# Kernel optimization log

Hardware: AMD Instinct MI355X
Metric: run time of the kernel (lower is better)

Reference implementation:

```python
import jax, jax.numpy as jnp
import numpy as np

B, T, D, O = 4, 1024, 256, 256


def setup_inputs() -> dict:
    key = jax.random.key(0)
    kx, kw = jax.random.split(key)
    x = jax.random.normal(kx, (B, T, D), dtype=jnp.float32)
    # he_normal init: stddev = sqrt(2 / fan_in), stacked per-position kernels [T, D, O]
    W = jax.random.normal(kw, (T, D, O), dtype=jnp.float32) * np.sqrt(2.0 / D).astype(np.float32)
    return {"x": x, "W": W}


def reference(x, W):
    # Original loop: out[:, i, :] = mean_{t<=i} (x[:, t, :] @ W[i])
    # = (cumulative mean of x along T) @ per-position kernel W[i].
    t = x.shape[1]
    counts = jnp.arange(1, t + 1, dtype=x.dtype)[:, None]  # (T,1)
    cm = jnp.cumsum(x, axis=1) / counts                    # (B,T,D) cumulative mean
    return jnp.einsum('btd,tdo->bto', cm, W)               # (B,T,O)
```

## Files before the change

kernel.cpp:

```cpp
#include <hip/hip_runtime.h>

#define B_ 4
#define T_ 1024
#define D_ 256
#define O_ 256
#define NC 32
#define CL 32

__global__ __launch_bounds__(256) void chunk_sums(const float* __restrict__ x,
                                                  float* __restrict__ S) {
    const int d  = threadIdx.x;
    const int bc = blockIdx.x;
    const int b  = bc / NC;
    const int c  = bc % NC;
    const float* xp = x + ((size_t)b * T_ + (size_t)c * CL) * D_ + d;
    float s = 0.f;
#pragma unroll
    for (int i = 0; i < CL; ++i) s += xp[(size_t)i * D_];
    S[((size_t)b * NC + c) * D_ + d] = s;
}

__global__ __launch_bounds__(256) void cumsum_mean(const float* __restrict__ x,
                                                   const float* __restrict__ S,
                                                   float* __restrict__ cm) {
    const int d  = threadIdx.x;
    const int bc = blockIdx.x;
    const int b  = bc / NC;
    const int c  = bc % NC;
    float off = 0.f;
    for (int cc = 0; cc < c; ++cc) off += S[((size_t)b * NC + cc) * D_ + d];
    const float* xp = x  + ((size_t)b * T_ + (size_t)c * CL) * D_ + d;
    float*       cp = cm + ((size_t)b * T_ + (size_t)c * CL) * D_ + d;
    float run = off;
#pragma unroll 4
    for (int i = 0; i < CL; ++i) {
        run += xp[(size_t)i * D_];
        const int t = c * CL + i;
        cp[(size_t)i * D_] = run / (float)(t + 1);
    }
}

__global__ __launch_bounds__(256) void gemm_t(const float* __restrict__ cm,
                                              const float* __restrict__ W,
                                              float* __restrict__ out) {
    const int t   = blockIdx.x;
    const int tid = threadIdx.x;
    const int oq  = tid & 63;
    const int dc  = tid >> 6;

    __shared__ float cml[D_][4];
    __shared__ float red[4][64][17];

#pragma unroll
    for (int b = 0; b < 4; ++b)
        cml[tid][b] = cm[((size_t)b * T_ + t) * D_ + tid];
    __syncthreads();

    const float* Wp = W + ((size_t)t * D_ + (size_t)dc * 64) * O_ + (size_t)oq * 4;

    float4 a0 = make_float4(0.f, 0.f, 0.f, 0.f);
    float4 a1 = a0, a2 = a0, a3 = a0;

#pragma unroll 8
    for (int i = 0; i < 64; ++i) {
        const float4 w  = *(const float4*)(Wp + (size_t)i * O_);
        const float4 c4 = *(const float4*)cml[dc * 64 + i];
        a0.x += c4.x * w.x; a0.y += c4.x * w.y; a0.z += c4.x * w.z; a0.w += c4.x * w.w;
        a1.x += c4.y * w.x; a1.y += c4.y * w.y; a1.z += c4.y * w.z; a1.w += c4.y * w.w;
        a2.x += c4.z * w.x; a2.y += c4.z * w.y; a2.z += c4.z * w.z; a2.w += c4.z * w.w;
        a3.x += c4.w * w.x; a3.y += c4.w * w.y; a3.z += c4.w * w.z; a3.w += c4.w * w.w;
    }

    float* r = red[dc][oq];
    r[ 0] = a0.x; r[ 1] = a0.y; r[ 2] = a0.z; r[ 3] = a0.w;
    r[ 4] = a1.x; r[ 5] = a1.y; r[ 6] = a1.z; r[ 7] = a1.w;
    r[ 8] = a2.x; r[ 9] = a2.y; r[10] = a2.z; r[11] = a2.w;
    r[12] = a3.x; r[13] = a3.y; r[14] = a3.z; r[15] = a3.w;
    __syncthreads();

    if (tid < 64) {
        float v[16];
#pragma unroll
        for (int k = 0; k < 16; ++k)
            v[k] = red[0][tid][k] + red[1][tid][k] + red[2][tid][k] + red[3][tid][k];
#pragma unroll
        for (int b = 0; b < 4; ++b) {
            float4 o4 = make_float4(v[b * 4 + 0], v[b * 4 + 1], v[b * 4 + 2], v[b * 4 + 3]);
            *(float4*)&out[((size_t)b * T_ + t) * O_ + (size_t)tid * 4] = o4;
        }
    }
}

extern "C" void kernel_launch(void* const* d_in, const int* in_sizes, int n_in,
                              void* d_out, int out_size, void* d_ws, size_t ws_size,
                              hipStream_t stream) {
    const float* x = (const float*)d_in[0];
    const float* W = (const float*)d_in[1];
    float* out = (float*)d_out;

    float* cm = (float*)d_ws;
    float* S  = (float*)d_ws + (size_t)B_ * T_ * D_;

    chunk_sums <<<B_ * NC, 256, 0, stream>>>(x, S);
    cumsum_mean<<<B_ * NC, 256, 0, stream>>>(x, S, cm);
    gemm_t     <<<T_,      256, 0, stream>>>(cm, W, out);
}
```

Before: 374.3 us.

## Restructure per-position GEMM: one wavefront per timestep, double-buffered nontemporal W loads

The GEMM kernel now gives each 64-thread wavefront a whole timestep over the full D reduction, with four timesteps per block. This removes the shared-memory cross-wave reduction and its second barrier. Weight rows are software-pipelined through a 16-register double buffer using nontemporal loads, and outputs are written with nontemporal stores. The cumsum offset loop is fully unrolled with predication. The cost is more register pressure and a grid of only 256 blocks, which may limit latency hiding on a bandwidth-bound 256 MB weight stream.

```diff
diff --git a/kernel.cpp b/kernel.cpp
--- a/kernel.cpp
+++ b/kernel.cpp
@@ -6,6 +6,8 @@
 #define O_ 256
 #define NC 32
 #define CL 32
+
+typedef float v4f __attribute__((ext_vector_type(4)));
 
 __global__ __launch_bounds__(256) void chunk_sums(const float* __restrict__ x,
                                                   float* __restrict__ S) {
@@ -28,7 +30,11 @@
     const int b  = bc / NC;
     const int c  = bc % NC;
     float off = 0.f;
-    for (int cc = 0; cc < c; ++cc) off += S[((size_t)b * NC + cc) * D_ + d];
+#pragma unroll
+    for (int cc = 0; cc < NC; ++cc) {
+        const float v = S[((size_t)b * NC + cc) * D_ + d];
+        off += (cc < c) ? v : 0.f;
+    }
     const float* xp = x  + ((size_t)b * T_ + (size_t)c * CL) * D_ + d;
     float*       cp = cm + ((size_t)b * T_ + (size_t)c * CL) * D_ + d;
     float run = off;
@@ -43,52 +49,57 @@
 __global__ __launch_bounds__(256) void gemm_t(const float* __restrict__ cm,
                                               const float* __restrict__ W,
                                               float* __restrict__ out) {
-    const int t   = blockIdx.x;
+    const int t0  = blockIdx.x * 4;
     const int tid = threadIdx.x;
+    const int tq  = tid >> 6;
     const int oq  = tid & 63;
-    const int dc  = tid >> 6;
 
-    __shared__ float cml[D_][4];
-    __shared__ float red[4][64][17];
+    __shared__ float cml[4][D_][4];
 
 #pragma unroll
-    for (int b = 0; b < 4; ++b)
-        cml[tid][b] = cm[((size_t)b * T_ + t) * D_ + tid];
+    for (int q = 0; q < 4; ++q)
+#pragma unroll
+        for (int b = 0; b < 4; ++b)
+            cml[q][tid][b] = cm[((size_t)b * T_ + t0 + q) * D_ + tid];
     __syncthreads();
 
-    const float* Wp = W + ((size_t)t * D_ + (size_t)dc * 64) * O_ + (size_t)oq * 4;
+    const v4f* Wp = (const v4f*)(W + (size_t)(t0 + tq) * D_ * O_) + oq;
 
-    float4 a0 = make_float4(0.f, 0.f, 0.f, 0.f);
-    float4 a1 = a0, a2 = a0, a3 = a0;
+    v4f a0 = (v4f)(0.f), a1 = (v4f)(0.f), a2 = (v4f)(0.f), a3 = (v4f)(0.f);
 
-#pragma unroll 8
-    for (int i = 0; i < 64; ++i) {
-        const float4 w  = *(const float4*)(Wp + (size_t)i * O_);
-        const float4 c4 = *(const float4*)cml[dc * 64 + i];
-        a0.x += c4.x * w.x; a0.y += c4.x * w.y; a0.z += c4.x * w.z; a0.w += c4.x * w.w;
-        a1.x += c4.y * w.x; a1.y += c4.y * w.y; a1.z += c4.y * w.z; a1.w += c4.y * w.w;
-        a2.x += c4.z * w.x; a2.y += c4.z * w.y; a2.z += c4.z * w.z; a2.w += c4.z * w.w;
-        a3.x += c4.w * w.x; a3.y += c4.w * w.y; a3.z += c4.w * w.z; a3.w += c4.w * w.w;
+    v4f w[16];
+#pragma unroll
+    for (int j = 0; j < 8; ++j)
+        w[j] = __builtin_nontemporal_load(Wp + (size_t)j * (O_ / 4));
+
+#pragma unroll 1
+    for (int dd = 0; dd < D_; dd += 16) {
+#pragma unroll
+        for (int j = 0; j < 8; ++j)
+            w[8 + j] = __builtin_nontemporal_load(Wp + (size_t)(dd + 8 + j) * (O_ / 4));
+#pragma unroll
+        for (int j = 0; j < 8; ++j) {
+            const v4f c4 = *(const v4f*)cml[tq][dd + j];
+            a0 += c4.x * w[j]; a1 += c4.y * w[j]; a2 += c4.z * w[j]; a3 += c4.w * w[j];
+        }
+        if (dd + 16 < D_) {
+#pragma unroll
+            for (int j = 0; j < 8; ++j)
+                w[j] = __builtin_nontemporal_load(Wp + (size_t)(dd + 16 + j) * (O_ / 4));
+        }
+#pragma unroll
+        for (int j = 0; j < 8; ++j) {
+            const v4f c4 = *(const v4f*)cml[tq][dd + 8 + j];
+            a0 += c4.x * w[8 + j]; a1 += c4.y * w[8 + j];
+            a2 += c4.z * w[8 + j]; a3 += c4.w * w[8 + j];
+        }
     }
 
-    float* r = red[dc][oq];
-    r[ 0] = a0.x; r[ 1] = a0.y; r[ 2] = a0.z; r[ 3] = a0.w;
-    r[ 4] = a1.x; r[ 5] = a1.y; r[ 6] = a1.z; r[ 7] = a1.w;
-    r[ 8] = a2.x; r[ 9] = a2.y; r[10] = a2.z; r[11] = a2.w;
-    r[12] = a3.x; r[13] = a3.y; r[14] = a3.z; r[15] = a3.w;
-    __syncthreads();
-
-    if (tid < 64) {
-        float v[16];
-#pragma unroll
-        for (int k = 0; k < 16; ++k)
-            v[k] = red[0][tid][k] + red[1][tid][k] + red[2][tid][k] + red[3][tid][k];
-#pragma unroll
-        for (int b = 0; b < 4; ++b) {
-            float4 o4 = make_float4(v[b * 4 + 0], v[b * 4 + 1], v[b * 4 + 2], v[b * 4 + 3]);
-            *(float4*)&out[((size_t)b * T_ + t) * O_ + (size_t)tid * 4] = o4;
-        }
-    }
+    const size_t obase = (size_t)(t0 + tq) * O_ + (size_t)oq * 4;
+    __builtin_nontemporal_store(a0, (v4f*)&out[(size_t)0 * T_ * O_ + obase]);
+    __builtin_nontemporal_store(a1, (v4f*)&out[(size_t)1 * T_ * O_ + obase]);
+    __builtin_nontemporal_store(a2, (v4f*)&out[(size_t)2 * T_ * O_ + obase]);
+    __builtin_nontemporal_store(a3, (v4f*)&out[(size_t)3 * T_ * O_ + obase]);
 }
 
 extern "C" void kernel_launch(void* const* d_in, const int* in_sizes, int n_in,
@@ -103,5 +114,5 @@
 
     chunk_sums <<<B_ * NC, 256, 0, stream>>>(x, S);
     cumsum_mean<<<B_ * NC, 256, 0, stream>>>(x, S, cm);
-    gemm_t     <<<T_,      256, 0, stream>>>(cm, W, out);
+    gemm_t     <<<T_ / 4,  256, 0, stream>>>(cm, W, out);
 }
```

Result: faster. 343.9 us (-8.1%).
